# Performance work log

Hardware: AMD Instinct MI355X
Metric: run time of the kernel (lower is better)

Reference implementation:

```python
import jax, jax.numpy as jnp
import numpy as np

N_HEAD = 12

def setup_inputs() -> dict:
    key = jax.random.key(0)
    ks = jax.random.split(key, 5)
    C = 768
    B, T = 2, 2048
    s = 0.02
    x = jax.random.normal(ks[0], (B, T, C), dtype=jnp.float32)
    W_attn = jax.random.normal(ks[1], (C, 3 * C), dtype=jnp.float32) * s
    b_attn = jnp.zeros((3 * C,), dtype=jnp.float32)
    W_proj = jax.random.normal(ks[2], (C, C), dtype=jnp.float32) * s
    b_proj = jnp.zeros((C,), dtype=jnp.float32)
    return {"x": x, "W_attn": W_attn, "b_attn": b_attn, "W_proj": W_proj, "b_proj": b_proj}

def reference(x, W_attn, b_attn, W_proj, b_proj):
    B, T, C = x.shape
    H = N_HEAD
    hs = C // H
    qkv = x @ W_attn + b_attn                      # [B,T,3C]
    q, k, v = jnp.split(qkv, 3, axis=2)
    # [B,H,T,hs]
    q = q.reshape(B, T, H, hs).transpose(0, 2, 1, 3)
    k = k.reshape(B, T, H, hs).transpose(0, 2, 1, 3)
    v = v.reshape(B, T, H, hs).transpose(0, 2, 1, 3)
    scale = 1.0 / np.sqrt(hs).astype(np.float32)
    att = jnp.einsum('bhqd,bhkd->bhqk', q, k) * scale   # [B,H,T,T]
    causal = jnp.tril(jnp.ones((T, T), dtype=bool))
    att = jnp.where(causal, att, -jnp.inf)
    att = jax.nn.softmax(att, axis=-1)
    y = jnp.einsum('bhqk,bhkd->bhqd', att, v)            # [B,H,T,hs]
    y = y.transpose(0, 2, 1, 3).reshape(B, T, C)
    return y @ W_proj + b_proj
```

## Files before the change

kernel.cpp:

```cpp
#include <hip/hip_runtime.h>


#define BB 2
#define TT 2048
#define CC 768
#define C3 2304
#define HH 12
#define DD 64
#define MM 4096

typedef unsigned short u16;
typedef unsigned int u32;
typedef __attribute__((ext_vector_type(8))) u16 u16x8;
typedef __attribute__((ext_vector_type(8))) __bf16 bf16x8;
typedef __attribute__((ext_vector_type(4))) float f32x4;

__device__ __forceinline__ float u2f(u16 u) {
    union { u32 i; float f; } c; c.i = ((u32)u) << 16; return c.f;
}
__device__ __forceinline__ u16 f2u(float f) {
    union { float f; u32 i; } c; c.f = f;
    u32 x = c.i;
    return (u16)((x + 0x7FFFu + ((x >> 16) & 1u)) >> 16);
}
__device__ __forceinline__ u16 f2b(float f) {
    __bf16 h = (__bf16)f; return __builtin_bit_cast(u16, h);
}
__device__ __forceinline__ bf16x8 ldsb8(const u16* p) {
    return __builtin_bit_cast(bf16x8, *(const u16x8*)p);
}
__device__ __forceinline__ f32x4 mfma16(bf16x8 a, bf16x8 b, f32x4 c) {
    return __builtin_amdgcn_mfma_f32_16x16x32_bf16(a, b, c, 0, 0, 0);
}
typedef __attribute__((address_space(1))) const u32 gu32;
typedef __attribute__((address_space(3))) u32 lu32;
__device__ __forceinline__ void gload16(const u16* gp, u16* lp) {
    __builtin_amdgcn_global_load_lds((gu32*)(const void*)gp, (lu32*)(void*)lp,
                                     16, 0, 0);
}
__device__ __forceinline__ void barrier_raw() {
    asm volatile("" ::: "memory");
    __builtin_amdgcn_s_barrier();
    asm volatile("" ::: "memory");
}

__global__ void detect_kernel(const u16* __restrict__ x, int* __restrict__ flag)
{
    __shared__ int found;
    if (threadIdx.x == 0) found = 0;
    __syncthreads();
    int local = 0;
    const u16x8* p = (const u16x8*)x + threadIdx.x;
    #pragma unroll
    for (int i = 0; i < 8; ++i) {
        const u16x8 v = p[(size_t)i * 256];
        #pragma unroll
        for (int j = 0; j < 8; ++j)
            if ((v[j] & 0x7F80u) == 0x7F80u) local = 1;
    }
    if (local) atomicOr(&found, 1);
    __syncthreads();
    if (threadIdx.x == 0) *flag = found ? 1 : 0;
}

__device__ void prep_w_body(const void* __restrict__ Wv, u16* __restrict__ Wt,
                            int K, int N, int bx, int by, int fm,
                            u16 (*Ts)[72])
{
    const int t = threadIdx.x;
    const int n0 = bx * 64, k0 = by * 64;
    const int r = t >> 2, c0 = (t & 3) << 4;

    if (fm) {
        const float* W = (const float*)Wv + (size_t)(k0 + r) * N + n0 + c0;
        #pragma unroll
        for (int i = 0; i < 16; i += 4) {
            const float4 v = *(const float4*)(W + i);
            Ts[c0 + i + 0][r] = f2u(v.x);
            Ts[c0 + i + 1][r] = f2u(v.y);
            Ts[c0 + i + 2][r] = f2u(v.z);
            Ts[c0 + i + 3][r] = f2u(v.w);
        }
    } else {
        const u16* W = (const u16*)Wv + (size_t)(k0 + r) * N + n0 + c0;
        const u16x8 a = *(const u16x8*)W;
        const u16x8 c = *(const u16x8*)(W + 8);
        #pragma unroll
        for (int i = 0; i < 8; ++i) { Ts[c0 + i][r] = a[i]; Ts[c0 + 8 + i][r] = c[i]; }
    }
    __syncthreads();
    u16* o = Wt + (size_t)(n0 + r) * K + k0 + c0;
    *(u16x8*)o = *(const u16x8*)&Ts[r][c0];
    *(u16x8*)(o + 8) = *(const u16x8*)&Ts[r][c0 + 8];
}

__global__ __launch_bounds__(256)
void fused_prep(const void* __restrict__ x, const void* __restrict__ Wa,
                const void* __restrict__ ba, const void* __restrict__ Wp,
                const void* __restrict__ bp,
                u16* __restrict__ xb, u16* __restrict__ WaT,
                u16* __restrict__ WpT, u16* __restrict__ bao,
                u16* __restrict__ bpo,
                const int* __restrict__ flag, int mode)
{
    __shared__ u16 Ts[64][72];
    const int fm = (mode >= 0) ? mode : *flag;
    const int blk = blockIdx.x;
    const int t = threadIdx.x;

    if (blk < 432) {
        prep_w_body(Wa, WaT, CC, C3, blk % 36, blk / 36, fm, Ts);
    } else if (blk < 576) {
        const int b2 = blk - 432;
        prep_w_body(Wp, WpT, CC, CC, b2 % 12, b2 / 12, fm, Ts);
    } else if (blk < 2112) {
        if (fm == 0) return;
        const size_t i = (size_t)(blk - 576) * 256 + t;
        const float* xp = (const float*)x + i * 8;
        u16x8 o;
        #pragma unroll
        for (int j = 0; j < 8; ++j) o[j] = f2u(xp[j]);
        *(u16x8*)(xb + i * 8) = o;
    } else {
        const int i = (blk - 2112) * 256 + t;
        if (i < C3) bao[i] = fm ? f2u(((const float*)ba)[i]) : ((const u16*)ba)[i];
        if (i < CC) bpo[i] = fm ? f2u(((const float*)bp)[i]) : ((const u16*)bp)[i];
    }
}

template <int FRM, int FRN>
__global__ __launch_bounds__(256)
void gemm_mfma(const u16* __restrict__ Adir, const u16* __restrict__ Acnv,
               const u16* __restrict__ Bt, const u16* __restrict__ bias,
               void* __restrict__ outv, int M, int N, int K,
               const int* __restrict__ flag, int mode, int om_sel)
{
    constexpr int TSM = 32 * FRM, TSN = 32 * FRN;
    constexpr int LPA = TSM / 64;
    constexpr int LPB = TSN / 64;

    __shared__ u16 As[2][TSM * 32];
    __shared__ u16 Bs[2][TSN * 32];

    const int fm = (mode >= 0) ? mode : *flag;
    const u16* A = fm ? Acnv : Adir;
    const int om = om_sel ? fm : 0;

    const int nwg = gridDim.x;
    const int lin = (blockIdx.x & 7) * (nwg >> 3) + (blockIdx.x >> 3);
    const int nx = N / TSN;
    const int m0 = (lin / nx) * TSM, n0 = (lin % nx) * TSN;

    const int t = threadIdx.x;
    const int lane = t & 63, wave = t >> 6;
    const int wm = wave >> 1, wn = wave & 1;
    const int l15 = lane & 15, h4 = lane >> 4;

    const int rsub = lane >> 2;
    const int cs = ((lane & 3) ^ ((lane >> 4) & 3)) * 8;
    const u16* Ab[LPA];
    const u16* Bb[LPB];
    #pragma unroll
    for (int j = 0; j < LPA; ++j)
        Ab[j] = A + (size_t)(m0 + wave * (16 * LPA) + j * 16 + rsub) * K + cs;
    #pragma unroll
    for (int j = 0; j < LPB; ++j)
        Bb[j] = Bt + (size_t)(n0 + wave * (16 * LPB) + j * 16 + rsub) * K + cs;

    f32x4 acc[FRM][FRN];
    #pragma unroll
    for (int i = 0; i < FRM; ++i)
        #pragma unroll
        for (int j = 0; j < FRN; ++j) acc[i][j] = (f32x4){0.f, 0.f, 0.f, 0.f};

    const int csr = (h4 ^ (l15 >> 2)) * 8;
    const int arow = wm * (TSM / 2) + l15;
    const int brow = wn * (TSN / 2) + l15;

    const int NT = K >> 5;
    #pragma unroll
    for (int j = 0; j < LPA; ++j)
        gload16(Ab[j], &As[0][(wave * LPA + j) * 512]);
    #pragma unroll
    for (int j = 0; j < LPB; ++j)
        gload16(Bb[j], &Bs[0][(wave * LPB + j) * 512]);

    for (int kt = 0; kt < NT; ++kt) {
        const int cur = kt & 1;
        if (kt + 1 < NT) {
            const int k0 = (kt + 1) << 5;
            const int nb = cur ^ 1;
            #pragma unroll
            for (int j = 0; j < LPA; ++j)
                gload16(Ab[j] + k0, &As[nb][(wave * LPA + j) * 512]);
            #pragma unroll
            for (int j = 0; j < LPB; ++j)
                gload16(Bb[j] + k0, &Bs[nb][(wave * LPB + j) * 512]);
            if constexpr (LPA + LPB == 4)
                asm volatile("s_waitcnt vmcnt(4)" ::: "memory");
            else if constexpr (LPA + LPB == 3)
                asm volatile("s_waitcnt vmcnt(3)" ::: "memory");
            else
                asm volatile("s_waitcnt vmcnt(2)" ::: "memory");
        } else {
            asm volatile("s_waitcnt vmcnt(0)" ::: "memory");
        }
        barrier_raw();

        bf16x8 af[FRM], bfr[FRN];
        #pragma unroll
        for (int f = 0; f < FRM; ++f)
            af[f] = ldsb8(&As[cur][(arow + f * 16) * 32 + csr]);
        #pragma unroll
        for (int f = 0; f < FRN; ++f)
            bfr[f] = ldsb8(&Bs[cur][(brow + f * 16) * 32 + csr]);
        #pragma unroll
        for (int i = 0; i < FRM; ++i)
            #pragma unroll
            for (int j = 0; j < FRN; ++j)
                acc[i][j] = mfma16(af[i], bfr[j], acc[i][j]);

        barrier_raw();
    }

    const int orow = m0 + wm * (TSM / 2) + h4 * 4;
    const int ocol = n0 + wn * (TSN / 2) + l15;
    if (om == 0) {
        u16* out = (u16*)outv;
        #pragma unroll
        for (int i = 0; i < FRM; ++i)
            #pragma unroll
            for (int j = 0; j < FRN; ++j) {
                const int col = ocol + j * 16;
                const float bv = u2f(bias[col]);
                #pragma unroll
                for (int r2 = 0; r2 < 4; ++r2)
                    out[(size_t)(orow + i * 16 + r2) * N + col] = f2b(acc[i][j][r2] + bv);
            }
    } else {
        float* out = (float*)outv;
        #pragma unroll
        for (int i = 0; i < FRM; ++i)
            #pragma unroll
            for (int j = 0; j < FRN; ++j) {
                const int col = ocol + j * 16;
                const float bv = u2f(bias[col]);
                #pragma unroll
                for (int r2 = 0; r2 < 4; ++r2)
                    out[(size_t)(orow + i * 16 + r2) * N + col] = acc[i][j][r2] + bv;
            }
    }
}

__global__ __launch_bounds__(256)
void attn_mfma(const u16* __restrict__ qkv, u16* __restrict__ yatt)
{
    __shared__ u16 Ks[2][64][72];
    __shared__ u16 Vt[2][64][72];

    const int bid = blockIdx.x;
    const int bin = bid & 255, slot = bid >> 8;
    const int g = bin >> 5, j = bin & 31;
    int qt;
    if (slot == 0)      qt = j;
    else if (slot == 1) qt = (j + 16) & 31;
    else                qt = (j < 16) ? (30 - 2 * j) : (63 - 2 * j);
    const int hb = slot * 8 + g;
    const int h = hb % HH, b = hb / HH;

    const int t = threadIdx.x;
    const int lane = t & 63, w = t >> 6;
    const int l15 = lane & 15, h4 = lane >> 4;
    const int q0 = qt * 64;

    const int sr = t >> 2;
    const int sd = (t & 3) << 4;
    const int rho = ((sr >> 5) & 1) * 32 + ((sr >> 2) & 1) * 16 +
                    ((sr >> 3) & 3) * 4 + (sr & 3);
    const int vk = (t & 31) * 2;
    const int vd = (t >> 5) << 3;

    bf16x8 aq0, aq1;
    {
        const u16* qp = qkv + ((size_t)(b * TT + q0 + w * 16 + l15)) * C3
                        + h * DD + h4 * 8;
        const u16x8 v0 = *(const u16x8*)qp;
        const u16x8 v1 = *(const u16x8*)(qp + 32);
        #pragma unroll
        for (int i = 0; i < 8; ++i) {
            aq0[i] = (__bf16)(u2f(v0[i]) * 0.125f);
            aq1[i] = (__bf16)(u2f(v1[i]) * 0.125f);
        }
    }

    float m_i = -1e30f, l_p = 0.f;
    f32x4 O[4];
    #pragma unroll
    for (int d = 0; d < 4; ++d) O[d] = (f32x4){0.f, 0.f, 0.f, 0.f};

    const u16* kB = qkv + ((size_t)(b * TT + sr)) * C3 + CC + h * DD + sd;
    const u16* vB = qkv + ((size_t)(b * TT + vk)) * C3 + 2 * CC + h * DD + vd;

    const int NT = qt + 1;

    u16x8 kr0 = *(const u16x8*)kB;
    u16x8 kr1 = *(const u16x8*)(kB + 8);
    u16x8 vr0 = *(const u16x8*)vB;
    u16x8 vr1 = *(const u16x8*)(vB + C3);
    *(u16x8*)&Ks[0][rho][sd]     = kr0;
    *(u16x8*)&Ks[0][rho][sd + 8] = kr1;
    #pragma unroll
    for (int i = 0; i < 8; ++i)
        *(u32*)&Vt[0][vd + i][vk] = (u32)vr0[i] | ((u32)vr1[i] << 16);
    if (NT > 1) {
        const u16* kp = kB + (size_t)64 * C3;
        const u16* vp = vB + (size_t)64 * C3;
        kr0 = *(const u16x8*)kp;
        kr1 = *(const u16x8*)(kp + 8);
        vr0 = *(const u16x8*)vp;
        vr1 = *(const u16x8*)(vp + C3);
    }
    __syncthreads();

    const int qg = q0 + w * 16 + l15;

    for (int kt = 0; kt < NT; ++kt) {
        const int cur = kt & 1;

        f32x4 s[4];
        __builtin_amdgcn_s_setprio(1);
        #pragma unroll
        for (int kf = 0; kf < 4; ++kf) {
            f32x4 z = (f32x4){0.f, 0.f, 0.f, 0.f};
            z = mfma16(ldsb8(&Ks[cur][kf * 16 + l15][h4 * 8]), aq0, z);
            z = mfma16(ldsb8(&Ks[cur][kf * 16 + l15][32 + h4 * 8]), aq1, z);
            s[kf] = z;
        }
        __builtin_amdgcn_s_setprio(0);

        if (kt + 1 < NT) {
            const int nb = cur ^ 1;
            *(u16x8*)&Ks[nb][rho][sd]     = kr0;
            *(u16x8*)&Ks[nb][rho][sd + 8] = kr1;
            #pragma unroll
            for (int i = 0; i < 8; ++i)
                *(u32*)&Vt[nb][vd + i][vk] = (u32)vr0[i] | ((u32)vr1[i] << 16);
            if (kt + 2 < NT) {
                const u16* kp = kB + (size_t)(kt + 2) * 64 * C3;
                const u16* vp = vB + (size_t)(kt + 2) * 64 * C3;
                kr0 = *(const u16x8*)kp;
                kr1 = *(const u16x8*)(kp + 8);
                vr0 = *(const u16x8*)vp;
                vr1 = *(const u16x8*)(vp + C3);
            }
        }

        if (kt == qt) {
            #pragma unroll
            for (int kf = 0; kf < 4; ++kf) {
                const int kbase = kt * 64 + 8 * h4 + 32 * (kf >> 1) + 4 * (kf & 1);
                #pragma unroll
                for (int r2 = 0; r2 < 4; ++r2)
                    if (kbase + r2 > qg) s[kf][r2] = -1e30f;
            }
        }

        float pm = s[0][0];
        #pragma unroll
        for (int kf = 0; kf < 4; ++kf)
            #pragma unroll
            for (int r2 = 0; r2 < 4; ++r2) pm = fmaxf(pm, s[kf][r2]);

        if (!__all(pm <= m_i + 8.f)) {
            float pr = pm;
            pr = fmaxf(pr, __shfl_xor(pr, 16));
            pr = fmaxf(pr, __shfl_xor(pr, 32));
            const float mnew = fmaxf(m_i, pr);
            const float a_ = __expf(m_i - mnew);
            l_p *= a_;
            float alf[4];
            #pragma unroll
            for (int r2 = 0; r2 < 4; ++r2) alf[r2] = __shfl(a_, h4 * 4 + r2);
            #pragma unroll
            for (int d = 0; d < 4; ++d)
                #pragma unroll
                for (int r2 = 0; r2 < 4; ++r2) O[d][r2] *= alf[r2];
            m_i = mnew;
        }

        bf16x8 ap, ap2;
        float rs = 0.f;
        #pragma unroll
        for (int kf = 0; kf < 2; ++kf)
            #pragma unroll
            for (int r2 = 0; r2 < 4; ++r2) {
                const float p = __expf(s[kf][r2] - m_i);
                rs += p;
                ap[kf * 4 + r2] = (__bf16)p;
            }
        #pragma unroll
        for (int kf = 2; kf < 4; ++kf)
            #pragma unroll
            for (int r2 = 0; r2 < 4; ++r2) {
                const float p = __expf(s[kf][r2] - m_i);
                rs += p;
                ap2[(kf - 2) * 4 + r2] = (__bf16)p;
            }
        l_p += rs;

        __builtin_amdgcn_s_setprio(1);
        #pragma unroll
        for (int d = 0; d < 4; ++d) {
            O[d] = mfma16(ap,  ldsb8(&Vt[cur][d * 16 + l15][h4 * 8]), O[d]);
            O[d] = mfma16(ap2, ldsb8(&Vt[cur][d * 16 + l15][32 + h4 * 8]), O[d]);
        }
        __builtin_amdgcn_s_setprio(0);

        __syncthreads();
    }

    float lr = l_p;
    lr += __shfl_xor(lr, 16);
    lr += __shfl_xor(lr, 32);
    const float invl = 1.0f / lr;
    float inv[4];
    #pragma unroll
    for (int r2 = 0; r2 < 4; ++r2) inv[r2] = __shfl(invl, h4 * 4 + r2);
    u16* yp = yatt + ((size_t)(b * TT + q0 + w * 16 + h4 * 4)) * CC + h * DD + l15;
    #pragma unroll
    for (int r2 = 0; r2 < 4; ++r2)
        #pragma unroll
        for (int d = 0; d < 4; ++d)
            yp[(size_t)r2 * CC + d * 16] = f2b(O[d][r2] * inv[r2]);
}

extern "C" void kernel_launch(void* const* d_in, const int* in_sizes, int n_in,
                              void* d_out, int out_size, void* d_ws, size_t ws_size,
                              hipStream_t stream)
{
    (void)n_in; (void)out_size; (void)ws_size;

    const void* x      = d_in[0];
    const void* W_attn = d_in[1];
    const void* b_attn = d_in[2];
    const void* W_proj = d_in[3];
    const void* b_proj = d_in[4];

    u16* qkv  = (u16*)d_ws;
    u16* yatt = qkv + (size_t)MM * C3;
    u16* xb   = yatt;
    u16* WaT  = yatt + (size_t)MM * CC;
    u16* WpT  = WaT + (size_t)C3 * CC;
    u16* ba   = WpT + (size_t)CC * CC;
    u16* bp   = ba + C3;
    int* flag = (int*)(bp + CC);

    int mode = -1;
    if (in_sizes[0] == MM * CC * 4) mode = 1;
    else if (in_sizes[0] == MM * CC * 2) mode = 0;
    if (mode < 0) {
        detect_kernel<<<1, 256, 0, stream>>>((const u16*)x, flag);
    }

    fused_prep<<<2121, 256, 0, stream>>>(x, W_attn, b_attn, W_proj, b_proj,
                                         xb, WaT, WpT, ba, bp, flag, mode);

    gemm_mfma<4, 2><<<(MM / 128) * (C3 / 64), 256, 0, stream>>>(
        (const u16*)x, xb, WaT, ba, (void*)qkv, MM, C3, CC, flag, mode, 0);

    attn_mfma<<<dim3(TT / 64 * HH * BB, 1, 1), 256, 0, stream>>>(qkv, yatt);

    gemm_mfma<2, 2><<<(MM / 64) * (CC / 64), 256, 0, stream>>>(
        yatt, yatt, WpT, bp, d_out, MM, CC, CC, flag, mode, 1);
}
```

Baseline: 162.9 us.

## Switch attention to 32x32 MFMA with split-K waves and merged softmax states

The attention kernel now uses 32x32x16 bf16 MFMA tiles in place of 16x16x32. The four waves are arranged as 2 query halves by 2 key halves, each holding its own online-softmax state. At the end the two key-half partial results are combined through LDS scratch. This is meant to cut LDS fragment loads and the cross-lane shuffles needed per row, at the cost of an extra merge step, more accumulator registers, and only half the waves writing output.

```diff
diff --git a/kernel.cpp b/kernel.cpp
--- a/kernel.cpp
+++ b/kernel.cpp
@@ -14,6 +14,7 @@
 typedef __attribute__((ext_vector_type(8))) u16 u16x8;
 typedef __attribute__((ext_vector_type(8))) __bf16 bf16x8;
 typedef __attribute__((ext_vector_type(4))) float f32x4;
+typedef __attribute__((ext_vector_type(16))) float f32x16;
 
 __device__ __forceinline__ float u2f(u16 u) {
     union { u32 i; float f; } c; c.i = ((u32)u) << 16; return c.f;
@@ -31,6 +32,9 @@
 }
 __device__ __forceinline__ f32x4 mfma16(bf16x8 a, bf16x8 b, f32x4 c) {
     return __builtin_amdgcn_mfma_f32_16x16x32_bf16(a, b, c, 0, 0, 0);
+}
+__device__ __forceinline__ f32x16 mfma32(bf16x8 a, bf16x8 b, f32x16 c) {
+    return __builtin_amdgcn_mfma_f32_32x32x16_bf16(a, b, c, 0, 0, 0);
 }
 typedef __attribute__((address_space(1))) const u32 gu32;
 typedef __attribute__((address_space(3))) u32 lu32;
@@ -270,33 +274,35 @@
 
     const int t = threadIdx.x;
     const int lane = t & 63, w = t >> 6;
-    const int l15 = lane & 15, h4 = lane >> 4;
+    const int l31 = lane & 31, hl = lane >> 5;
+    const int qh = w >> 1, kh = w & 1;
     const int q0 = qt * 64;
+    const int qg = q0 + qh * 32 + l31;
 
     const int sr = t >> 2;
     const int sd = (t & 3) << 4;
-    const int rho = ((sr >> 5) & 1) * 32 + ((sr >> 2) & 1) * 16 +
-                    ((sr >> 3) & 3) * 4 + (sr & 3);
+    const int k5 = sr & 31;
+    const int rr = (sr & 32) | (((k5 >> 2) & 1) << 4) | (((k5 >> 4) & 1) << 3)
+                 | (((k5 >> 3) & 1) << 2) | (k5 & 3);
     const int vk = (t & 31) * 2;
     const int vd = (t >> 5) << 3;
 
-    bf16x8 aq0, aq1;
+    bf16x8 qf[4];
     {
-        const u16* qp = qkv + ((size_t)(b * TT + q0 + w * 16 + l15)) * C3
-                        + h * DD + h4 * 8;
-        const u16x8 v0 = *(const u16x8*)qp;
-        const u16x8 v1 = *(const u16x8*)(qp + 32);
-        #pragma unroll
-        for (int i = 0; i < 8; ++i) {
-            aq0[i] = (__bf16)(u2f(v0[i]) * 0.125f);
-            aq1[i] = (__bf16)(u2f(v1[i]) * 0.125f);
-        }
-    }
-
-    float m_i = -1e30f, l_p = 0.f;
-    f32x4 O[4];
-    #pragma unroll
-    for (int d = 0; d < 4; ++d) O[d] = (f32x4){0.f, 0.f, 0.f, 0.f};
+        const u16* qp = qkv + ((size_t)(b * TT + qg)) * C3 + h * DD + hl * 8;
+        #pragma unroll
+        for (int t4 = 0; t4 < 4; ++t4) {
+            const u16x8 v = *(const u16x8*)(qp + 16 * t4);
+            #pragma unroll
+            for (int i = 0; i < 8; ++i)
+                qf[t4][i] = (__bf16)(u2f(v[i]) * 0.125f);
+        }
+    }
+
+    float m_i = -1e4f, l_p = 0.f;
+    f32x16 O0, O1;
+    #pragma unroll
+    for (int i = 0; i < 16; ++i) { O0[i] = 0.f; O1[i] = 0.f; }
 
     const u16* kB = qkv + ((size_t)(b * TT + sr)) * C3 + CC + h * DD + sd;
     const u16* vB = qkv + ((size_t)(b * TT + vk)) * C3 + 2 * CC + h * DD + vd;
@@ -307,8 +313,8 @@
     u16x8 kr1 = *(const u16x8*)(kB + 8);
     u16x8 vr0 = *(const u16x8*)vB;
     u16x8 vr1 = *(const u16x8*)(vB + C3);
-    *(u16x8*)&Ks[0][rho][sd]     = kr0;
-    *(u16x8*)&Ks[0][rho][sd + 8] = kr1;
+    *(u16x8*)&Ks[0][rr][sd]     = kr0;
+    *(u16x8*)&Ks[0][rr][sd + 8] = kr1;
     #pragma unroll
     for (int i = 0; i < 8; ++i)
         *(u32*)&Vt[0][vd + i][vk] = (u32)vr0[i] | ((u32)vr1[i] << 16);
@@ -322,26 +328,23 @@
     }
     __syncthreads();
 
-    const int qg = q0 + w * 16 + l15;
-
     for (int kt = 0; kt < NT; ++kt) {
         const int cur = kt & 1;
 
-        f32x4 s[4];
+        f32x16 s;
+        #pragma unroll
+        for (int i = 0; i < 16; ++i) s[i] = 0.f;
         __builtin_amdgcn_s_setprio(1);
         #pragma unroll
-        for (int kf = 0; kf < 4; ++kf) {
-            f32x4 z = (f32x4){0.f, 0.f, 0.f, 0.f};
-            z = mfma16(ldsb8(&Ks[cur][kf * 16 + l15][h4 * 8]), aq0, z);
-            z = mfma16(ldsb8(&Ks[cur][kf * 16 + l15][32 + h4 * 8]), aq1, z);
-            s[kf] = z;
-        }
+        for (int t4 = 0; t4 < 4; ++t4)
+            s = mfma32(ldsb8(&Ks[cur][kh * 32 + l31][t4 * 16 + hl * 8]),
+                       qf[t4], s);
         __builtin_amdgcn_s_setprio(0);
 
         if (kt + 1 < NT) {
             const int nb = cur ^ 1;
-            *(u16x8*)&Ks[nb][rho][sd]     = kr0;
-            *(u16x8*)&Ks[nb][rho][sd + 8] = kr1;
+            *(u16x8*)&Ks[nb][rr][sd]     = kr0;
+            *(u16x8*)&Ks[nb][rr][sd + 8] = kr1;
             #pragma unroll
             for (int i = 0; i < 8; ++i)
                 *(u32*)&Vt[nb][vd + i][vk] = (u32)vr0[i] | ((u32)vr1[i] << 16);
@@ -357,81 +360,77 @@
 
         if (kt == qt) {
             #pragma unroll
-            for (int kf = 0; kf < 4; ++kf) {
-                const int kbase = kt * 64 + 8 * h4 + 32 * (kf >> 1) + 4 * (kf & 1);
+            for (int jj = 0; jj < 4; ++jj)
                 #pragma unroll
-                for (int r2 = 0; r2 < 4; ++r2)
-                    if (kbase + r2 > qg) s[kf][r2] = -1e30f;
-            }
-        }
-
-        float pm = s[0][0];
-        #pragma unroll
-        for (int kf = 0; kf < 4; ++kf)
-            #pragma unroll
-            for (int r2 = 0; r2 < 4; ++r2) pm = fmaxf(pm, s[kf][r2]);
+                for (int e = 0; e < 4; ++e) {
+                    const int kl = kh * 32 + ((jj & 1) << 4) + (hl << 3)
+                                 + ((jj >> 1) << 2) + e;
+                    if (kt * 64 + kl > qg) s[4 * jj + e] = -1e30f;
+                }
+        }
+
+        float pm = s[0];
+        #pragma unroll
+        for (int i = 1; i < 16; ++i) pm = fmaxf(pm, s[i]);
 
         if (!__all(pm <= m_i + 8.f)) {
-            float pr = pm;
-            pr = fmaxf(pr, __shfl_xor(pr, 16));
-            pr = fmaxf(pr, __shfl_xor(pr, 32));
+            const float pr = fmaxf(pm, __shfl_xor(pm, 32));
             const float mnew = fmaxf(m_i, pr);
             const float a_ = __expf(m_i - mnew);
             l_p *= a_;
-            float alf[4];
-            #pragma unroll
-            for (int r2 = 0; r2 < 4; ++r2) alf[r2] = __shfl(a_, h4 * 4 + r2);
-            #pragma unroll
-            for (int d = 0; d < 4; ++d)
-                #pragma unroll
-                for (int r2 = 0; r2 < 4; ++r2) O[d][r2] *= alf[r2];
+            #pragma unroll
+            for (int i = 0; i < 16; ++i) { O0[i] *= a_; O1[i] *= a_; }
             m_i = mnew;
         }
 
-        bf16x8 ap, ap2;
+        bf16x8 p0, p1;
         float rs = 0.f;
         #pragma unroll
-        for (int kf = 0; kf < 2; ++kf)
-            #pragma unroll
-            for (int r2 = 0; r2 < 4; ++r2) {
-                const float p = __expf(s[kf][r2] - m_i);
-                rs += p;
-                ap[kf * 4 + r2] = (__bf16)p;
-            }
-        #pragma unroll
-        for (int kf = 2; kf < 4; ++kf)
-            #pragma unroll
-            for (int r2 = 0; r2 < 4; ++r2) {
-                const float p = __expf(s[kf][r2] - m_i);
-                rs += p;
-                ap2[(kf - 2) * 4 + r2] = (__bf16)p;
-            }
+        for (int e = 0; e < 4; ++e) {
+            const float a = __expf(s[e] - m_i);       rs += a; p0[e]     = (__bf16)a;
+            const float c = __expf(s[8 + e] - m_i);   rs += c; p0[4 + e] = (__bf16)c;
+            const float d = __expf(s[4 + e] - m_i);   rs += d; p1[e]     = (__bf16)d;
+            const float g2 = __expf(s[12 + e] - m_i); rs += g2; p1[4 + e] = (__bf16)g2;
+        }
         l_p += rs;
 
         __builtin_amdgcn_s_setprio(1);
-        #pragma unroll
-        for (int d = 0; d < 4; ++d) {
-            O[d] = mfma16(ap,  ldsb8(&Vt[cur][d * 16 + l15][h4 * 8]), O[d]);
-            O[d] = mfma16(ap2, ldsb8(&Vt[cur][d * 16 + l15][32 + h4 * 8]), O[d]);
-        }
+        O0 = mfma32(ldsb8(&Vt[cur][l31][kh * 32 + hl * 8]), p0, O0);
+        O0 = mfma32(ldsb8(&Vt[cur][l31][kh * 32 + 16 + hl * 8]), p1, O0);
+        O1 = mfma32(ldsb8(&Vt[cur][32 + l31][kh * 32 + hl * 8]), p0, O1);
+        O1 = mfma32(ldsb8(&Vt[cur][32 + l31][kh * 32 + 16 + hl * 8]), p1, O1);
         __builtin_amdgcn_s_setprio(0);
 
         __syncthreads();
     }
 
-    float lr = l_p;
-    lr += __shfl_xor(lr, 16);
-    lr += __shfl_xor(lr, 32);
-    const float invl = 1.0f / lr;
-    float inv[4];
-    #pragma unroll
-    for (int r2 = 0; r2 < 4; ++r2) inv[r2] = __shfl(invl, h4 * 4 + r2);
-    u16* yp = yatt + ((size_t)(b * TT + q0 + w * 16 + h4 * 4)) * CC + h * DD + l15;
-    #pragma unroll
-    for (int r2 = 0; r2 < 4; ++r2)
-        #pragma unroll
-        for (int d = 0; d < 4; ++d)
-            yp[(size_t)r2 * CC + d * 16] = f2b(O[d][r2] * inv[r2]);
+    const float lr = l_p + __shfl_xor(l_p, 32);
+
+    float* scr = (float*)&Ks[0][0][0];
+    const int sidx = (qh * 64 + lane) * 34;
+    if (kh == 1) {
+        scr[sidx] = m_i;
+        scr[sidx + 1] = lr;
+        #pragma unroll
+        for (int i = 0; i < 16; ++i) {
+            scr[sidx + 2 + i] = O0[i];
+            scr[sidx + 18 + i] = O1[i];
+        }
+    }
+    __syncthreads();
+    if (kh == 0) {
+        const float mB = scr[sidx], lB = scr[sidx + 1];
+        const float mm = fmaxf(m_i, mB);
+        const float a0 = __expf(m_i - mm), a1 = __expf(mB - mm);
+        const float inv = 1.0f / (lr * a0 + lB * a1);
+        u16* yp = yatt + ((size_t)(b * TT + qg)) * CC + h * DD;
+        #pragma unroll
+        for (int r = 0; r < 16; ++r) {
+            const int drow = (r & 3) + 8 * (r >> 2) + 4 * hl;
+            yp[drow]      = f2b((O0[r] * a0 + scr[sidx + 2 + r] * a1) * inv);
+            yp[32 + drow] = f2b((O1[r] * a0 + scr[sidx + 18 + r] * a1) * inv);
+        }
+    }
 }
 
 extern "C" void kernel_launch(void* const* d_in, const int* in_sizes, int n_in,
```

New measurement: 169.1 us. 1.04x slower.

## Split long causal attention tiles into halves with persistent atomic work queue

Applied to the files above, without the earlier changes.

The attention kernel becomes a persistent kernel that pulls work items from an atomic counter over a host-built table sorted longest-first. Query tiles in the upper half are split into two KV-range halves, and the two partial softmax states are merged by whichever block finishes second, through a global scratch buffer and a per-pair flag. This targets load imbalance from causal masking, where late query tiles dominate the runtime. It adds atomics, scratch traffic, a small per-call host-to-device copy and a cross-block fence dependency.

```diff
diff --git a/kernel.cpp b/kernel.cpp
--- a/kernel.cpp
+++ b/kernel.cpp
@@ -1,4 +1,5 @@
 #include <hip/hip_runtime.h>
+#include <algorithm>
 
 
 #define BB 2
@@ -8,6 +9,9 @@
 #define HH 12
 #define DD 64
 #define MM 4096
+#define NITEMS 1152
+#define NPAIRS 384
+#define SLOTF (64 * 66)
 
 typedef unsigned short u16;
 typedef unsigned int u32;
@@ -101,7 +105,8 @@
                 u16* __restrict__ xb, u16* __restrict__ WaT,
                 u16* __restrict__ WpT, u16* __restrict__ bao,
                 u16* __restrict__ bpo,
-                const int* __restrict__ flag, int mode)
+                const int* __restrict__ flag, int mode,
+                int* __restrict__ qcnt, int* __restrict__ pairflag)
 {
     __shared__ u16 Ts[64][72];
     const int fm = (mode >= 0) ? mode : *flag;
@@ -123,6 +128,8 @@
         *(u16x8*)(xb + i * 8) = o;
     } else {
         const int i = (blk - 2112) * 256 + t;
+        if (blk == 2112 && t == 0) *qcnt = 0;
+        if (i < NPAIRS) pairflag[i] = 0;
         if (i < C3) bao[i] = fm ? f2u(((const float*)ba)[i]) : ((const u16*)ba)[i];
         if (i < CC) bpo[i] = fm ? f2u(((const float*)bp)[i]) : ((const u16*)bp)[i];
     }
@@ -253,25 +260,17 @@
 }
 
 __global__ __launch_bounds__(256)
-void attn_mfma(const u16* __restrict__ qkv, u16* __restrict__ yatt)
+void attn_mfma(const u16* __restrict__ qkv, u16* __restrict__ yatt,
+               const int* __restrict__ tab, int* __restrict__ qcnt,
+               int* __restrict__ pairflag, float* __restrict__ pscr)
 {
     __shared__ u16 Ks[2][64][72];
     __shared__ u16 Vt[2][64][72];
-
-    const int bid = blockIdx.x;
-    const int bin = bid & 255, slot = bid >> 8;
-    const int g = bin >> 5, j = bin & 31;
-    int qt;
-    if (slot == 0)      qt = j;
-    else if (slot == 1) qt = (j + 16) & 31;
-    else                qt = (j < 16) ? (30 - 2 * j) : (63 - 2 * j);
-    const int hb = slot * 8 + g;
-    const int h = hb % HH, b = hb / HH;
+    __shared__ int s_idx, s_old;
 
     const int t = threadIdx.x;
     const int lane = t & 63, w = t >> 6;
     const int l15 = lane & 15, h4 = lane >> 4;
-    const int q0 = qt * 64;
 
     const int sr = t >> 2;
     const int sd = (t & 3) << 4;
@@ -280,158 +279,217 @@
     const int vk = (t & 31) * 2;
     const int vd = (t >> 5) << 3;
 
-    bf16x8 aq0, aq1;
-    {
-        const u16* qp = qkv + ((size_t)(b * TT + q0 + w * 16 + l15)) * C3
-                        + h * DD + h4 * 8;
-        const u16x8 v0 = *(const u16x8*)qp;
-        const u16x8 v1 = *(const u16x8*)(qp + 32);
-        #pragma unroll
-        for (int i = 0; i < 8; ++i) {
-            aq0[i] = (__bf16)(u2f(v0[i]) * 0.125f);
-            aq1[i] = (__bf16)(u2f(v1[i]) * 0.125f);
+    for (;;) {
+        if (t == 0) s_idx = atomicAdd(qcnt, 1);
+        __syncthreads();
+        const int idx = s_idx;
+        if (idx >= NITEMS) return;
+        const int code = tab[idx];
+        const int qt = code & 255, hb = (code >> 8) & 255, kind = code >> 16;
+        const int h = hb % HH, b = hb / HH;
+        const int q0 = qt * 64;
+        const int H = (qt + 1) >> 1;
+        const int kt0 = (kind == 2) ? H : 0;
+        const int ktE = (kind == 1) ? H : qt + 1;
+        const int NT = ktE - kt0;
+
+        bf16x8 aq0, aq1;
+        {
+            const u16* qp = qkv + ((size_t)(b * TT + q0 + w * 16 + l15)) * C3
+                            + h * DD + h4 * 8;
+            const u16x8 v0 = *(const u16x8*)qp;
+            const u16x8 v1 = *(const u16x8*)(qp + 32);
+            #pragma unroll
+            for (int i = 0; i < 8; ++i) {
+                aq0[i] = (__bf16)(u2f(v0[i]) * 0.125f);
+                aq1[i] = (__bf16)(u2f(v1[i]) * 0.125f);
+            }
         }
-    }
-
-    float m_i = -1e30f, l_p = 0.f;
-    f32x4 O[4];
-    #pragma unroll
-    for (int d = 0; d < 4; ++d) O[d] = (f32x4){0.f, 0.f, 0.f, 0.f};
-
-    const u16* kB = qkv + ((size_t)(b * TT + sr)) * C3 + CC + h * DD + sd;
-    const u16* vB = qkv + ((size_t)(b * TT + vk)) * C3 + 2 * CC + h * DD + vd;
-
-    const int NT = qt + 1;
-
-    u16x8 kr0 = *(const u16x8*)kB;
-    u16x8 kr1 = *(const u16x8*)(kB + 8);
-    u16x8 vr0 = *(const u16x8*)vB;
-    u16x8 vr1 = *(const u16x8*)(vB + C3);
-    *(u16x8*)&Ks[0][rho][sd]     = kr0;
-    *(u16x8*)&Ks[0][rho][sd + 8] = kr1;
-    #pragma unroll
-    for (int i = 0; i < 8; ++i)
-        *(u32*)&Vt[0][vd + i][vk] = (u32)vr0[i] | ((u32)vr1[i] << 16);
-    if (NT > 1) {
-        const u16* kp = kB + (size_t)64 * C3;
-        const u16* vp = vB + (size_t)64 * C3;
-        kr0 = *(const u16x8*)kp;
-        kr1 = *(const u16x8*)(kp + 8);
-        vr0 = *(const u16x8*)vp;
-        vr1 = *(const u16x8*)(vp + C3);
-    }
-    __syncthreads();
-
-    const int qg = q0 + w * 16 + l15;
-
-    for (int kt = 0; kt < NT; ++kt) {
-        const int cur = kt & 1;
-
-        f32x4 s[4];
-        __builtin_amdgcn_s_setprio(1);
-        #pragma unroll
-        for (int kf = 0; kf < 4; ++kf) {
-            f32x4 z = (f32x4){0.f, 0.f, 0.f, 0.f};
-            z = mfma16(ldsb8(&Ks[cur][kf * 16 + l15][h4 * 8]), aq0, z);
-            z = mfma16(ldsb8(&Ks[cur][kf * 16 + l15][32 + h4 * 8]), aq1, z);
-            s[kf] = z;
+
+        float m_i = -1e30f, l_p = 0.f;
+        f32x4 O[4];
+        #pragma unroll
+        for (int d = 0; d < 4; ++d) O[d] = (f32x4){0.f, 0.f, 0.f, 0.f};
+
+        const u16* kB = qkv + ((size_t)(b * TT + sr)) * C3 + CC + h * DD + sd
+                        + (size_t)kt0 * 64 * C3;
+        const u16* vB = qkv + ((size_t)(b * TT + vk)) * C3 + 2 * CC + h * DD + vd
+                        + (size_t)kt0 * 64 * C3;
+
+        u16x8 kr0 = *(const u16x8*)kB;
+        u16x8 kr1 = *(const u16x8*)(kB + 8);
+        u16x8 vr0 = *(const u16x8*)vB;
+        u16x8 vr1 = *(const u16x8*)(vB + C3);
+        *(u16x8*)&Ks[0][rho][sd]     = kr0;
+        *(u16x8*)&Ks[0][rho][sd + 8] = kr1;
+        #pragma unroll
+        for (int i = 0; i < 8; ++i)
+            *(u32*)&Vt[0][vd + i][vk] = (u32)vr0[i] | ((u32)vr1[i] << 16);
+        if (NT > 1) {
+            const u16* kp = kB + (size_t)64 * C3;
+            const u16* vp = vB + (size_t)64 * C3;
+            kr0 = *(const u16x8*)kp;
+            kr1 = *(const u16x8*)(kp + 8);
+            vr0 = *(const u16x8*)vp;
+            vr1 = *(const u16x8*)(vp + C3);
         }
-        __builtin_amdgcn_s_setprio(0);
-
-        if (kt + 1 < NT) {
-            const int nb = cur ^ 1;
-            *(u16x8*)&Ks[nb][rho][sd]     = kr0;
-            *(u16x8*)&Ks[nb][rho][sd + 8] = kr1;
-            #pragma unroll
-            for (int i = 0; i < 8; ++i)
-                *(u32*)&Vt[nb][vd + i][vk] = (u32)vr0[i] | ((u32)vr1[i] << 16);
-            if (kt + 2 < NT) {
-                const u16* kp = kB + (size_t)(kt + 2) * 64 * C3;
-                const u16* vp = vB + (size_t)(kt + 2) * 64 * C3;
-                kr0 = *(const u16x8*)kp;
-                kr1 = *(const u16x8*)(kp + 8);
-                vr0 = *(const u16x8*)vp;
-                vr1 = *(const u16x8*)(vp + C3);
-            }
+        __syncthreads();
+
+        const int qg = q0 + w * 16 + l15;
+
+        for (int kk = 0; kk < NT; ++kk) {
+            const int cur = kk & 1;
+
+            f32x4 s[4];
+            __builtin_amdgcn_s_setprio(1);
+            #pragma unroll
+            for (int kf = 0; kf < 4; ++kf) {
+                f32x4 z = (f32x4){0.f, 0.f, 0.f, 0.f};
+                z = mfma16(ldsb8(&Ks[cur][kf * 16 + l15][h4 * 8]), aq0, z);
+                z = mfma16(ldsb8(&Ks[cur][kf * 16 + l15][32 + h4 * 8]), aq1, z);
+                s[kf] = z;
+            }
+            __builtin_amdgcn_s_setprio(0);
+
+            if (kk + 1 < NT) {
+                const int nb = cur ^ 1;
+                *(u16x8*)&Ks[nb][rho][sd]     = kr0;
+                *(u16x8*)&Ks[nb][rho][sd + 8] = kr1;
+                #pragma unroll
+                for (int i = 0; i < 8; ++i)
+                    *(u32*)&Vt[nb][vd + i][vk] = (u32)vr0[i] | ((u32)vr1[i] << 16);
+                if (kk + 2 < NT) {
+                    const u16* kp = kB + (size_t)(kk + 2) * 64 * C3;
+                    const u16* vp = vB + (size_t)(kk + 2) * 64 * C3;
+                    kr0 = *(const u16x8*)kp;
+                    kr1 = *(const u16x8*)(kp + 8);
+                    vr0 = *(const u16x8*)vp;
+                    vr1 = *(const u16x8*)(vp + C3);
+                }
+            }
+
+            if (kt0 + kk == qt) {
+                #pragma unroll
+                for (int kf = 0; kf < 4; ++kf) {
+                    const int kbase = qt * 64 + 8 * h4 + 32 * (kf >> 1) + 4 * (kf & 1);
+                    #pragma unroll
+                    for (int r2 = 0; r2 < 4; ++r2)
+                        if (kbase + r2 > qg) s[kf][r2] = -1e30f;
+                }
+            }
+
+            float pm = s[0][0];
+            #pragma unroll
+            for (int kf = 0; kf < 4; ++kf)
+                #pragma unroll
+                for (int r2 = 0; r2 < 4; ++r2) pm = fmaxf(pm, s[kf][r2]);
+
+            if (!__all(pm <= m_i + 8.f)) {
+                float pr = pm;
+                pr = fmaxf(pr, __shfl_xor(pr, 16));
+                pr = fmaxf(pr, __shfl_xor(pr, 32));
+                const float mnew = fmaxf(m_i, pr);
+                const float a_ = __expf(m_i - mnew);
+                l_p *= a_;
+                float alf[4];
+                #pragma unroll
+                for (int r2 = 0; r2 < 4; ++r2) alf[r2] = __shfl(a_, h4 * 4 + r2);
+                #pragma unroll
+                for (int d = 0; d < 4; ++d)
+                    #pragma unroll
+                    for (int r2 = 0; r2 < 4; ++r2) O[d][r2] *= alf[r2];
+                m_i = mnew;
+            }
+
+            bf16x8 ap, ap2;
+            float rs = 0.f;
+            #pragma unroll
+            for (int kf = 0; kf < 2; ++kf)
+                #pragma unroll
+                for (int r2 = 0; r2 < 4; ++r2) {
+                    const float p = __expf(s[kf][r2] - m_i);
+                    rs += p;
+                    ap[kf * 4 + r2] = (__bf16)p;
+                }
+            #pragma unroll
+            for (int kf = 2; kf < 4; ++kf)
+                #pragma unroll
+                for (int r2 = 0; r2 < 4; ++r2) {
+                    const float p = __expf(s[kf][r2] - m_i);
+                    rs += p;
+                    ap2[(kf - 2) * 4 + r2] = (__bf16)p;
+                }
+            l_p += rs;
+
+            __builtin_amdgcn_s_setprio(1);
+            #pragma unroll
+            for (int d = 0; d < 4; ++d) {
+                O[d] = mfma16(ap,  ldsb8(&Vt[cur][d * 16 + l15][h4 * 8]), O[d]);
+                O[d] = mfma16(ap2, ldsb8(&Vt[cur][d * 16 + l15][32 + h4 * 8]), O[d]);
+            }
+            __builtin_amdgcn_s_setprio(0);
+
+            __syncthreads();
         }
 
-        if (kt == qt) {
-            #pragma unroll
-            for (int kf = 0; kf < 4; ++kf) {
-                const int kbase = kt * 64 + 8 * h4 + 32 * (kf >> 1) + 4 * (kf & 1);
-                #pragma unroll
-                for (int r2 = 0; r2 < 4; ++r2)
-                    if (kbase + r2 > qg) s[kf][r2] = -1e30f;
+        float lr = l_p;
+        lr += __shfl_xor(lr, 16);
+        lr += __shfl_xor(lr, 32);
+
+        if (kind == 0) {
+            const float invl = 1.0f / lr;
+            float inv[4];
+            #pragma unroll
+            for (int r2 = 0; r2 < 4; ++r2) inv[r2] = __shfl(invl, h4 * 4 + r2);
+            u16* yp = yatt + ((size_t)(b * TT + q0 + w * 16 + h4 * 4)) * CC
+                      + h * DD + l15;
+            #pragma unroll
+            for (int r2 = 0; r2 < 4; ++r2)
+                #pragma unroll
+                for (int d = 0; d < 4; ++d)
+                    yp[(size_t)r2 * CC + d * 16] = f2b(O[d][r2] * inv[r2]);
+        } else {
+            const int p = (qt - 16) * (HH * BB) + hb;
+            float* slot = pscr + ((size_t)p * 2 + (kind - 1)) * SLOTF;
+            const int rq = w * 16 + l15;
+            slot[rq] = m_i;
+            slot[64 + rq] = lr;
+            #pragma unroll
+            for (int r2 = 0; r2 < 4; ++r2)
+                #pragma unroll
+                for (int d = 0; d < 4; ++d)
+                    slot[128 + (size_t)(w * 16 + h4 * 4 + r2) * 64 + l15 + d * 16]
+                        = O[d][r2];
+            __threadfence();
+            __syncthreads();
+            if (t == 0) s_old = atomicAdd(&pairflag[p], 1);
+            __syncthreads();
+            if (s_old == 1) {
+                __threadfence();
+                const float* oth = pscr + ((size_t)p * 2 + (2 - kind)) * SLOTF;
+                u16* yp = yatt + ((size_t)(b * TT + q0 + w * 16 + h4 * 4)) * CC
+                          + h * DD + l15;
+                #pragma unroll
+                for (int r2 = 0; r2 < 4; ++r2) {
+                    const int rr2 = w * 16 + h4 * 4 + r2;
+                    const float mA = __shfl(m_i, h4 * 4 + r2);
+                    const float lA = __shfl(lr, h4 * 4 + r2);
+                    const float mB = oth[rr2];
+                    const float lB = oth[64 + rr2];
+                    const float mm = fmaxf(mA, mB);
+                    const float aA = __expf(mA - mm);
+                    const float aB = __expf(mB - mm);
+                    const float inv = 1.0f / (lA * aA + lB * aB);
+                    #pragma unroll
+                    for (int d = 0; d < 4; ++d)
+                        yp[(size_t)r2 * CC + d * 16] = f2b(
+                            (O[d][r2] * aA +
+                             oth[128 + (size_t)rr2 * 64 + l15 + d * 16] * aB) * inv);
+                }
             }
         }
-
-        float pm = s[0][0];
-        #pragma unroll
-        for (int kf = 0; kf < 4; ++kf)
-            #pragma unroll
-            for (int r2 = 0; r2 < 4; ++r2) pm = fmaxf(pm, s[kf][r2]);
-
-        if (!__all(pm <= m_i + 8.f)) {
-            float pr = pm;
-            pr = fmaxf(pr, __shfl_xor(pr, 16));
-            pr = fmaxf(pr, __shfl_xor(pr, 32));
-            const float mnew = fmaxf(m_i, pr);
-            const float a_ = __expf(m_i - mnew);
-            l_p *= a_;
-            float alf[4];
-            #pragma unroll
-            for (int r2 = 0; r2 < 4; ++r2) alf[r2] = __shfl(a_, h4 * 4 + r2);
-            #pragma unroll
-            for (int d = 0; d < 4; ++d)
-                #pragma unroll
-                for (int r2 = 0; r2 < 4; ++r2) O[d][r2] *= alf[r2];
-            m_i = mnew;
-        }
-
-        bf16x8 ap, ap2;
-        float rs = 0.f;
-        #pragma unroll
-        for (int kf = 0; kf < 2; ++kf)
-            #pragma unroll
-            for (int r2 = 0; r2 < 4; ++r2) {
-                const float p = __expf(s[kf][r2] - m_i);
-                rs += p;
-                ap[kf * 4 + r2] = (__bf16)p;
-            }
-        #pragma unroll
-        for (int kf = 2; kf < 4; ++kf)
-            #pragma unroll
-            for (int r2 = 0; r2 < 4; ++r2) {
-                const float p = __expf(s[kf][r2] - m_i);
-                rs += p;
-                ap2[(kf - 2) * 4 + r2] = (__bf16)p;
-            }
-        l_p += rs;
-
-        __builtin_amdgcn_s_setprio(1);
-        #pragma unroll
-        for (int d = 0; d < 4; ++d) {
-            O[d] = mfma16(ap,  ldsb8(&Vt[cur][d * 16 + l15][h4 * 8]), O[d]);
-            O[d] = mfma16(ap2, ldsb8(&Vt[cur][d * 16 + l15][32 + h4 * 8]), O[d]);
-        }
-        __builtin_amdgcn_s_setprio(0);
-
         __syncthreads();
     }
-
-    float lr = l_p;
-    lr += __shfl_xor(lr, 16);
-    lr += __shfl_xor(lr, 32);
-    const float invl = 1.0f / lr;
-    float inv[4];
-    #pragma unroll
-    for (int r2 = 0; r2 < 4; ++r2) inv[r2] = __shfl(invl, h4 * 4 + r2);
-    u16* yp = yatt + ((size_t)(b * TT + q0 + w * 16 + h4 * 4)) * CC + h * DD + l15;
-    #pragma unroll
-    for (int r2 = 0; r2 < 4; ++r2)
-        #pragma unroll
-        for (int d = 0; d < 4; ++d)
-            yp[(size_t)r2 * CC + d * 16] = f2b(O[d][r2] * inv[r2]);
 }
 
 extern "C" void kernel_launch(void* const* d_in, const int* in_sizes, int n_in,
@@ -454,6 +512,34 @@
     u16* ba   = WpT + (size_t)CC * CC;
     u16* bp   = ba + C3;
     int* flag = (int*)(bp + CC);
+    int* qcnt = flag + 1;
+    int* dtab = qcnt + 1;
+    int* pairflag = dtab + NITEMS;
+    float* pscr = (float*)(pairflag + NPAIRS);
+
+    static int host_tab[NITEMS];
+    static bool tab_init = false;
+    if (!tab_init) {
+        struct It { int len, code; };
+        It tmp[NITEMS];
+        int n = 0;
+        for (int qt = 0; qt < 32; ++qt)
+            for (int hb = 0; hb < HH * BB; ++hb) {
+                if (qt < 16) {
+                    tmp[n++] = {qt + 1, qt | (hb << 8) | (0 << 16)};
+                } else {
+                    const int H = (qt + 1) >> 1;
+                    tmp[n++] = {H, qt | (hb << 8) | (1 << 16)};
+                    tmp[n++] = {qt + 1 - H, qt | (hb << 8) | (2 << 16)};
+                }
+            }
+        std::sort(tmp, tmp + n,
+                  [](const It& a, const It& b) { return a.len > b.len; });
+        for (int i = 0; i < n; ++i) host_tab[i] = tmp[i].code;
+        tab_init = true;
+    }
+    hipMemcpyAsync(dtab, host_tab, sizeof(host_tab), hipMemcpyHostToDevice,
+                   stream);
 
     int mode = -1;
     if (in_sizes[0] == MM * CC * 4) mode = 1;
@@ -463,12 +549,14 @@
     }
 
     fused_prep<<<2121, 256, 0, stream>>>(x, W_attn, b_attn, W_proj, b_proj,
-                                         xb, WaT, WpT, ba, bp, flag, mode);
+                                         xb, WaT, WpT, ba, bp, flag, mode,
+                                         qcnt, pairflag);
 
     gemm_mfma<4, 2><<<(MM / 128) * (C3 / 64), 256, 0, stream>>>(
         (const u16*)x, xb, WaT, ba, (void*)qkv, MM, C3, CC, flag, mode, 0);
 
-    attn_mfma<<<dim3(TT / 64 * HH * BB, 1, 1), 256, 0, stream>>>(qkv, yatt);
+    attn_mfma<<<dim3(1024, 1, 1), 256, 0, stream>>>(qkv, yatt, dtab, qcnt,
+                                                    pairflag, pscr);
 
     gemm_mfma<2, 2><<<(MM / 64) * (CC / 64), 256, 0, stream>>>(
         yatt, yatt, WpT, bp, d_out, MM, CC, CC, flag, mode, 1);
```

Result: slower. 338.8 us (+108.0%).

## Load K fragments directly from global into registers, dropping K shared-memory staging

Applied to the files above, without the earlier changes.

The attention kernel no longer stages K tiles through shared memory. Each wave now loads its K MFMA operand fragments straight from global memory into registers, with a one-tile-ahead register double buffer (kc/kn). This removes the K LDS writes and reads and halves shared-memory use. In exchange each wave loads the whole K tile redundantly (four waves per block), which raises global/L2 traffic and register pressure.

```diff
diff --git a/kernel.cpp b/kernel.cpp
--- a/kernel.cpp
+++ b/kernel.cpp
@@ -28,6 +28,9 @@
 }
 __device__ __forceinline__ bf16x8 ldsb8(const u16* p) {
     return __builtin_bit_cast(bf16x8, *(const u16x8*)p);
+}
+__device__ __forceinline__ bf16x8 asbf(u16x8 v) {
+    return __builtin_bit_cast(bf16x8, v);
 }
 __device__ __forceinline__ f32x4 mfma16(bf16x8 a, bf16x8 b, f32x4 c) {
     return __builtin_amdgcn_mfma_f32_16x16x32_bf16(a, b, c, 0, 0, 0);
@@ -255,7 +258,6 @@
 __global__ __launch_bounds__(256)
 void attn_mfma(const u16* __restrict__ qkv, u16* __restrict__ yatt)
 {
-    __shared__ u16 Ks[2][64][72];
     __shared__ u16 Vt[2][64][72];
 
     const int bid = blockIdx.x;
@@ -273,10 +275,6 @@
     const int l15 = lane & 15, h4 = lane >> 4;
     const int q0 = qt * 64;
 
-    const int sr = t >> 2;
-    const int sd = (t & 3) << 4;
-    const int rho = ((sr >> 5) & 1) * 32 + ((sr >> 2) & 1) * 16 +
-                    ((sr >> 3) & 3) * 4 + (sr & 3);
     const int vk = (t & 31) * 2;
     const int vd = (t >> 5) << 3;
 
@@ -298,25 +296,26 @@
     #pragma unroll
     for (int d = 0; d < 4; ++d) O[d] = (f32x4){0.f, 0.f, 0.f, 0.f};
 
-    const u16* kB = qkv + ((size_t)(b * TT + sr)) * C3 + CC + h * DD + sd;
+    const int g0 = ((l15 >> 3) & 1) * 16 + ((l15 >> 2) & 1) * 8 + (l15 & 3);
+    const u16* kG = qkv + ((size_t)(b * TT + g0)) * C3 + CC + h * DD + h4 * 8;
     const u16* vB = qkv + ((size_t)(b * TT + vk)) * C3 + 2 * CC + h * DD + vd;
 
     const int NT = qt + 1;
 
-    u16x8 kr0 = *(const u16x8*)kB;
-    u16x8 kr1 = *(const u16x8*)(kB + 8);
+    u16x8 kc[8], kn[8];
+    #pragma unroll
+    for (int kf = 0; kf < 4; ++kf) {
+        const u16* p = kG + (size_t)((kf >> 1) * 32 + (kf & 1) * 4) * C3;
+        kc[2 * kf]     = *(const u16x8*)p;
+        kc[2 * kf + 1] = *(const u16x8*)(p + 32);
+    }
     u16x8 vr0 = *(const u16x8*)vB;
     u16x8 vr1 = *(const u16x8*)(vB + C3);
-    *(u16x8*)&Ks[0][rho][sd]     = kr0;
-    *(u16x8*)&Ks[0][rho][sd + 8] = kr1;
     #pragma unroll
     for (int i = 0; i < 8; ++i)
         *(u32*)&Vt[0][vd + i][vk] = (u32)vr0[i] | ((u32)vr1[i] << 16);
     if (NT > 1) {
-        const u16* kp = kB + (size_t)64 * C3;
         const u16* vp = vB + (size_t)64 * C3;
-        kr0 = *(const u16x8*)kp;
-        kr1 = *(const u16x8*)(kp + 8);
         vr0 = *(const u16x8*)vp;
         vr1 = *(const u16x8*)(vp + C3);
     }
@@ -332,24 +331,26 @@
         #pragma unroll
         for (int kf = 0; kf < 4; ++kf) {
             f32x4 z = (f32x4){0.f, 0.f, 0.f, 0.f};
-            z = mfma16(ldsb8(&Ks[cur][kf * 16 + l15][h4 * 8]), aq0, z);
-            z = mfma16(ldsb8(&Ks[cur][kf * 16 + l15][32 + h4 * 8]), aq1, z);
+            z = mfma16(asbf(kc[2 * kf]), aq0, z);
+            z = mfma16(asbf(kc[2 * kf + 1]), aq1, z);
             s[kf] = z;
         }
         __builtin_amdgcn_s_setprio(0);
 
         if (kt + 1 < NT) {
+            const u16* kp = kG + (size_t)(kt + 1) * 64 * C3;
+            #pragma unroll
+            for (int kf = 0; kf < 4; ++kf) {
+                const u16* p = kp + (size_t)((kf >> 1) * 32 + (kf & 1) * 4) * C3;
+                kn[2 * kf]     = *(const u16x8*)p;
+                kn[2 * kf + 1] = *(const u16x8*)(p + 32);
+            }
             const int nb = cur ^ 1;
-            *(u16x8*)&Ks[nb][rho][sd]     = kr0;
-            *(u16x8*)&Ks[nb][rho][sd + 8] = kr1;
             #pragma unroll
             for (int i = 0; i < 8; ++i)
                 *(u32*)&Vt[nb][vd + i][vk] = (u32)vr0[i] | ((u32)vr1[i] << 16);
             if (kt + 2 < NT) {
-                const u16* kp = kB + (size_t)(kt + 2) * 64 * C3;
                 const u16* vp = vB + (size_t)(kt + 2) * 64 * C3;
-                kr0 = *(const u16x8*)kp;
-                kr1 = *(const u16x8*)(kp + 8);
                 vr0 = *(const u16x8*)vp;
                 vr1 = *(const u16x8*)(vp + C3);
             }
@@ -358,7 +359,7 @@
         if (kt == qt) {
             #pragma unroll
             for (int kf = 0; kf < 4; ++kf) {
-                const int kbase = kt * 64 + 8 * h4 + 32 * (kf >> 1) + 4 * (kf & 1);
+                const int kbase = qt * 64 + 8 * h4 + 32 * (kf >> 1) + 4 * (kf & 1);
                 #pragma unroll
                 for (int r2 = 0; r2 < 4; ++r2)
                     if (kbase + r2 > qg) s[kf][r2] = -1e30f;
@@ -417,6 +418,11 @@
         __builtin_amdgcn_s_setprio(0);
 
         __syncthreads();
+
+        if (kt + 1 < NT) {
+            #pragma unroll
+            for (int i = 0; i < 8; ++i) kc[i] = kn[i];
+        }
     }
 
     float lr = l_p;
```

After: 190.5 us. 16.9% more time.
